# Kernel tuning notes

Hardware: AMD Instinct MI355X
Metric: run time of the kernel (lower is better)

Reference implementation:

```python
import jax, jax.numpy as jnp
import numpy as np
import math

D_IN = 1024
D_FEATURES = 4096
DEGREE = 4
BATCH = 16384


def fwht(x):
    """Unnormalized Fast Walsh-Hadamard transform along the last axis (size power of 2)."""
    n = x.shape[-1]
    orig = x.shape
    h = 1
    while h < n:
        # view as (..., n/(2h), 2, h): butterfly pairs of length-h blocks
        y = x.reshape(orig[:-1] + (n // (2 * h), 2, h))
        a = y[..., 0, :]
        b = y[..., 1, :]
        x = jnp.stack([a + b, a - b], axis=-2).reshape(orig)
        h *= 2
    return x


def setup_inputs() -> dict:
    key = jax.random.key(0)
    k_x, k_rad = jax.random.split(key)
    x = jax.random.normal(k_x, (BATCH, D_IN), dtype=jnp.float32)
    # Rademacher +-1 samples, shape (degree, d_in)
    rad = (2.0 * jax.random.randint(k_rad, (DEGREE, D_IN), 0, 2).astype(jnp.float32) - 1.0)
    # permutations exactly as in resample(): tile arange(d_in) num_blocks times, shuffle, take first d_features
    num_blocks = int(math.ceil(D_FEATURES / D_IN))
    rng = np.random.RandomState(0)
    perms = []
    for _ in range(DEGREE):
        indices = np.tile(np.arange(D_IN), num_blocks)
        perms.append(indices[rng.permutation(len(indices))][:D_FEATURES])
    permutations = jnp.asarray(np.stack(perms, axis=0), dtype=jnp.int32)
    log_lengthscale = jnp.full((1,), np.log(np.sqrt(D_IN)), dtype=jnp.float32)  # lengthscale='auto'
    log_var = jnp.zeros((1,), dtype=jnp.float32)  # var=1.0
    return {"x": x, "rad": rad, "permutations": permutations,
            "log_lengthscale": log_lengthscale, "log_var": log_var}


def reference(x, rad, permutations, log_lengthscale, log_var):
    B = x.shape[0]
    x = x / jnp.exp(log_lengthscale)            # [B, d_in]
    x = x[:, None, :] * rad                     # [B, degree, d_in]
    x = fwht(x)                                 # FWHT along d_in
    idx = jnp.broadcast_to(permutations[None], (B,) + permutations.shape)
    x = jnp.take_along_axis(x, idx, axis=2)     # [B, degree, d_features]
    x = jnp.prod(x, axis=1)                     # degree-wise product -> [B, d_features]
    x = x * jnp.exp(log_var / 2.0)
    return x / float(np.sqrt(D_FEATURES))
```

## Files before the change

### kernel.cpp

```cpp
#include <hip/hip_runtime.h>
#include <math.h>


#define D_IN_N 1024
#define D_FEAT 4096

template <int CTRL>
__device__ __forceinline__ float dpp_xor(float x) {
  int r = __builtin_amdgcn_mov_dpp(__float_as_int(x), CTRL, 0xF, 0xF, true);
  return __int_as_float(r);
}

__global__ __launch_bounds__(256, 4) void srht_kernel(
    const float* __restrict__ x,
    const float* __restrict__ rad,
    const int*  __restrict__ perms,
    const float* __restrict__ log_ls,
    const float* __restrict__ log_var,
    float* __restrict__ out)
{
  __shared__ float stage[4][64 * 17];
  __shared__ float ybuf[4][D_IN_N];

  const int tid = threadIdx.x;
  const int w = tid >> 6;
  const int l = tid & 63;
  const long long b = blockIdx.x;

  const float4* x4 = reinterpret_cast<const float4*>(x + b * D_IN_N);
  const float4* r4 = reinterpret_cast<const float4*>(rad + (long long)w * D_IN_N);
  float v[16];
#pragma unroll
  for (int q = 0; q < 4; ++q) {
    float4 xa = x4[l * 4 + q];
    float4 ra = r4[l * 4 + q];
    v[4 * q + 0] = xa.x * ra.x;
    v[4 * q + 1] = xa.y * ra.y;
    v[4 * q + 2] = xa.z * ra.z;
    v[4 * q + 3] = xa.w * ra.w;
  }
#pragma unroll
  for (int h = 1; h < 16; h <<= 1) {
#pragma unroll
    for (int m = 0; m < 16; ++m) {
      if (!(m & h)) {
        float va = v[m], vb = v[m + h];
        v[m] = va + vb;
        v[m + h] = va - vb;
      }
    }
  }

#pragma unroll
  for (int m = 0; m < 16; ++m) stage[w][l * 17 + m] = v[m];
  __syncthreads();

  const int c = l & 3;
  const int a = l >> 2;
#pragma unroll
  for (int m2 = 0; m2 < 16; ++m2) v[m2] = stage[w][(c + 4 * m2) * 17 + a];
#pragma unroll
  for (int h = 1; h < 16; h <<= 1) {
#pragma unroll
    for (int m = 0; m < 16; ++m) {
      if (!(m & h)) {
        float va = v[m], vb = v[m + h];
        v[m] = va + vb;
        v[m + h] = va - vb;
      }
    }
  }

#pragma unroll
  for (int m = 0; m < 16; ++m) {
    float o = dpp_xor<0xB1>(v[m]);
    v[m] = (l & 1) ? (o - v[m]) : (v[m] + o);
  }
#pragma unroll
  for (int m = 0; m < 16; ++m) {
    float o = dpp_xor<0x4E>(v[m]);
    v[m] = (l & 2) ? (o - v[m]) : (v[m] + o);
  }

#pragma unroll
  for (int m = 0; m < 16; ++m) ybuf[w][a + 16 * c + 64 * m] = v[m];
  __syncthreads();

  const float scale = expf(0.5f * log_var[0] - 4.0f * log_ls[0]) * (1.0f / 64.0f);

  const int4* pm = reinterpret_cast<const int4*>(perms);
  float4* out4 = reinterpret_cast<float4*>(out + b * D_FEAT);
#pragma unroll
  for (int seg = 0; seg < 4; ++seg) {
    int fi = seg * 256 + tid;
    int4 p0 = pm[0 * 1024 + fi];
    int4 p1 = pm[1 * 1024 + fi];
    int4 p2 = pm[2 * 1024 + fi];
    int4 p3 = pm[3 * 1024 + fi];
    float4 o;
    o.x = ybuf[0][p0.x] * ybuf[1][p1.x] * ybuf[2][p2.x] * ybuf[3][p3.x] * scale;
    o.y = ybuf[0][p0.y] * ybuf[1][p1.y] * ybuf[2][p2.y] * ybuf[3][p3.y] * scale;
    o.z = ybuf[0][p0.z] * ybuf[1][p1.z] * ybuf[2][p2.z] * ybuf[3][p3.z] * scale;
    o.w = ybuf[0][p0.w] * ybuf[1][p1.w] * ybuf[2][p2.w] * ybuf[3][p3.w] * scale;
    out4[fi] = o;
  }
}

extern "C" void kernel_launch(void* const* d_in, const int* in_sizes, int n_in,
                              void* d_out, int out_size, void* d_ws, size_t ws_size,
                              hipStream_t stream) {
  const float* x      = (const float*)d_in[0];
  const float* rad    = (const float*)d_in[1];
  const int*   perms  = (const int*)d_in[2];
  const float* lls    = (const float*)d_in[3];
  const float* lv     = (const float*)d_in[4];
  float* out          = (float*)d_out;

  const int batch = in_sizes[0] / D_IN_N;
  srht_kernel<<<batch, 256, 0, stream>>>(x, rad, perms, lls, lv, out);
}
```

Baseline: 364.2 us.

## Replace LDS transpose in FWHT with cross-lane DPP, swizzle and permlane32 butterflies

Changes the data layout so each lane holds elements strided by 64. The 1024-point FWHT is then done as 16-point butterflies in registers plus six cross-lane stages using DPP, ds_swizzle and permlane32_swap, with sign-selected FMAs. This drops the staging shared buffer and one barrier, and the freed LDS lets occupancy rise to 6 blocks per CU. The trade-offs are loads that are now scalar and strided instead of float4, ds_swizzle traffic through the LDS crossbar, and less unrolling in the gather loop.

Result: no change. 370.1 us (+1.6%).

```diff
diff --git a/kernel.cpp b/kernel.cpp
--- a/kernel.cpp
+++ b/kernel.cpp
@@ -5,13 +5,20 @@
 #define D_IN_N 1024
 #define D_FEAT 4096
 
+typedef unsigned uint2v __attribute__((ext_vector_type(2)));
+
 template <int CTRL>
 __device__ __forceinline__ float dpp_xor(float x) {
   int r = __builtin_amdgcn_mov_dpp(__float_as_int(x), CTRL, 0xF, 0xF, true);
   return __int_as_float(r);
 }
 
-__global__ __launch_bounds__(256, 4) void srht_kernel(
+template <int IMM>
+__device__ __forceinline__ float lds_swz(float x) {
+  return __int_as_float(__builtin_amdgcn_ds_swizzle(__float_as_int(x), IMM));
+}
+
+__global__ __launch_bounds__(256, 6) void srht_kernel(
     const float* __restrict__ x,
     const float* __restrict__ rad,
     const int*  __restrict__ perms,
@@ -19,7 +26,6 @@
     const float* __restrict__ log_var,
     float* __restrict__ out)
 {
-  __shared__ float stage[4][64 * 17];
   __shared__ float ybuf[4][D_IN_N];
 
   const int tid = threadIdx.x;
@@ -27,18 +33,19 @@
   const int l = tid & 63;
   const long long b = blockIdx.x;
 
-  const float4* x4 = reinterpret_cast<const float4*>(x + b * D_IN_N);
-  const float4* r4 = reinterpret_cast<const float4*>(rad + (long long)w * D_IN_N);
+  const float s0 = (l & 1)  ? -1.0f : 1.0f;
+  const float s1 = (l & 2)  ? -1.0f : 1.0f;
+  const float s2 = (l & 4)  ? -1.0f : 1.0f;
+  const float s3 = (l & 8)  ? -1.0f : 1.0f;
+  const float s4 = (l & 16) ? -1.0f : 1.0f;
+  const float s5 = (l & 32) ? -1.0f : 1.0f;
+
+  const float* xb = x + b * D_IN_N + l;
+  const float* rb = rad + (long long)w * D_IN_N + l;
   float v[16];
 #pragma unroll
-  for (int q = 0; q < 4; ++q) {
-    float4 xa = x4[l * 4 + q];
-    float4 ra = r4[l * 4 + q];
-    v[4 * q + 0] = xa.x * ra.x;
-    v[4 * q + 1] = xa.y * ra.y;
-    v[4 * q + 2] = xa.z * ra.z;
-    v[4 * q + 3] = xa.w * ra.w;
-  }
+  for (int m = 0; m < 16; ++m) v[m] = xb[m * 64] * rb[m * 64];
+
 #pragma unroll
   for (int h = 1; h < 16; h <<= 1) {
 #pragma unroll
@@ -52,45 +59,38 @@
   }
 
 #pragma unroll
-  for (int m = 0; m < 16; ++m) stage[w][l * 17 + m] = v[m];
-  __syncthreads();
+  for (int m = 0; m < 16; ++m) v[m] = fmaf(v[m], s0, dpp_xor<0xB1>(v[m]));
+#pragma unroll
+  for (int m = 0; m < 16; ++m) v[m] = fmaf(v[m], s1, dpp_xor<0x4E>(v[m]));
 
-  const int c = l & 3;
-  const int a = l >> 2;
 #pragma unroll
-  for (int m2 = 0; m2 < 16; ++m2) v[m2] = stage[w][(c + 4 * m2) * 17 + a];
+  for (int m = 0; m < 16; ++m) v[m] = fmaf(v[m], s2, lds_swz<0x101F>(v[m]));
 #pragma unroll
-  for (int h = 1; h < 16; h <<= 1) {
+  for (int m = 0; m < 16; ++m) v[m] = fmaf(v[m], s3, lds_swz<0x201F>(v[m]));
 #pragma unroll
-    for (int m = 0; m < 16; ++m) {
-      if (!(m & h)) {
-        float va = v[m], vb = v[m + h];
-        v[m] = va + vb;
-        v[m + h] = va - vb;
-      }
-    }
+  for (int m = 0; m < 16; ++m) v[m] = fmaf(v[m], s4, lds_swz<0x401F>(v[m]));
+
+#pragma unroll
+  for (int m = 0; m < 16; ++m) {
+    unsigned u = __float_as_uint(v[m]);
+    uint2v r = __builtin_amdgcn_permlane32_swap(u, u, false, false);
+    v[m] = fmaf(__uint_as_float(r.y), s5, __uint_as_float(r.x));
   }
 
 #pragma unroll
-  for (int m = 0; m < 16; ++m) {
-    float o = dpp_xor<0xB1>(v[m]);
-    v[m] = (l & 1) ? (o - v[m]) : (v[m] + o);
-  }
-#pragma unroll
-  for (int m = 0; m < 16; ++m) {
-    float o = dpp_xor<0x4E>(v[m]);
-    v[m] = (l & 2) ? (o - v[m]) : (v[m] + o);
-  }
-
-#pragma unroll
-  for (int m = 0; m < 16; ++m) ybuf[w][a + 16 * c + 64 * m] = v[m];
+  for (int m = 0; m < 16; ++m) ybuf[w][m * 64 + l] = v[m];
   __syncthreads();
 
   const float scale = expf(0.5f * log_var[0] - 4.0f * log_ls[0]) * (1.0f / 64.0f);
 
+  const float* __restrict__ y0 = ybuf[0];
+  const float* __restrict__ y1 = ybuf[1];
+  const float* __restrict__ y2 = ybuf[2];
+  const float* __restrict__ y3 = ybuf[3];
+
   const int4* pm = reinterpret_cast<const int4*>(perms);
   float4* out4 = reinterpret_cast<float4*>(out + b * D_FEAT);
-#pragma unroll
+#pragma unroll 2
   for (int seg = 0; seg < 4; ++seg) {
     int fi = seg * 256 + tid;
     int4 p0 = pm[0 * 1024 + fi];
@@ -98,10 +98,10 @@
     int4 p2 = pm[2 * 1024 + fi];
     int4 p3 = pm[3 * 1024 + fi];
     float4 o;
-    o.x = ybuf[0][p0.x] * ybuf[1][p1.x] * ybuf[2][p2.x] * ybuf[3][p3.x] * scale;
-    o.y = ybuf[0][p0.y] * ybuf[1][p1.y] * ybuf[2][p2.y] * ybuf[3][p3.y] * scale;
-    o.z = ybuf[0][p0.z] * ybuf[1][p1.z] * ybuf[2][p2.z] * ybuf[3][p3.z] * scale;
-    o.w = ybuf[0][p0.w] * ybuf[1][p1.w] * ybuf[2][p2.w] * ybuf[3][p3.w] * scale;
+    o.x = y0[p0.x] * y1[p1.x] * y2[p2.x] * y3[p3.x] * scale;
+    o.y = y0[p0.y] * y1[p1.y] * y2[p2.y] * y3[p3.y] * scale;
+    o.z = y0[p0.z] * y1[p1.z] * y2[p2.z] * y3[p3.z] * scale;
+    o.w = y0[p0.w] * y1[p1.w] * y2[p2.w] * y3[p3.w] * scale;
     out4[fi] = o;
   }
 }
```
